# Kernel optimization log

Measured on AMD Instinct MI355X. Metric: run time of the kernel, lower is better.

The kernel has to match this reference:

```python
import jax, jax.numpy as jnp
import numpy as np

B = 128          # graphs per batch
NP = 1024        # nodes per graph
FIN = 128        # input node features
H = 128          # hidden width (SAGEConv out)
C = 10           # output classes
N = B * NP
DEG = 16
E = N * DEG
K1 = int(np.ceil(0.8 * NP))   # 820
K2 = int(np.ceil(0.8 * K1))   # 656
K3 = int(np.ceil(0.8 * K2))   # 525


def setup_inputs() -> dict:
    key = jax.random.key(0)
    k = jax.random.split(key, 16)
    x = jax.random.normal(k[0], (N, FIN), jnp.float32)
    # edges constrained within each graph (PyG batched-graph semantics)
    g = jnp.arange(E, dtype=jnp.int32) // (E // B)
    src = g * NP + jax.random.randint(k[1], (E,), 0, NP, jnp.int32)
    dst = g * NP + jax.random.randint(k[2], (E,), 0, NP, jnp.int32)
    edge_index = jnp.stack([src, dst])

    def lin(kk, o, i):
        return jax.random.normal(kk, (o, i), jnp.float32) / np.sqrt(i)

    return {
        'x': x, 'edge_index': edge_index,
        'Wl1': lin(k[3], H, FIN), 'bl1': jnp.zeros((H,), jnp.float32), 'Wr1': lin(k[4], H, FIN),
        'wp1': jax.random.normal(k[5], (H,), jnp.float32),
        'Wl2': lin(k[6], H, H), 'bl2': jnp.zeros((H,), jnp.float32), 'Wr2': lin(k[7], H, H),
        'wp2': jax.random.normal(k[8], (H,), jnp.float32),
        'Wl3': lin(k[9], H, H), 'bl3': jnp.zeros((H,), jnp.float32), 'Wr3': lin(k[10], H, H),
        'wp3': jax.random.normal(k[11], (H,), jnp.float32),
        'Wf1': lin(k[12], 64, H), 'bf1': jnp.zeros((64,), jnp.float32),
        'Wf2': lin(k[13], C, 64), 'bf2': jnp.zeros((C,), jnp.float32),
    }


def _sage(x, src, dst, em, Wl, bl, Wr):
    # PyG SAGEConv: lin_l(mean_{j in N(i)} x_j) + lin_r(x_i); edge mask em kills pruned edges
    msg = x[src] * em[:, None]                                   # [E,H] gather
    s = jax.ops.segment_sum(msg, dst, num_segments=N)            # scatter-add
    deg = jax.ops.segment_sum(em, dst, num_segments=N)
    mean = s / jnp.maximum(deg, 1.0)[:, None]
    return mean @ Wl.T + bl + x @ Wr.T


def _topk(x, w, nm, kk):
    # TopKPooling: score = x.w/||w||, keep top ceil(ratio*n) per graph, gate kept nodes by tanh(score)
    score = (x @ w) / (jnp.linalg.norm(w) + 1e-16)               # [N]
    s2 = jnp.where(nm, score, -jnp.inf).reshape(B, NP)
    _, idx = jax.lax.top_k(s2, kk)                               # [B,kk] static shape
    sel = jnp.zeros((B, NP), bool).at[jnp.arange(B)[:, None], idx].set(True).reshape(-1)
    x = jnp.where(sel[:, None], x * jnp.tanh(score)[:, None], 0.0)
    return x, sel


def _forward(x, Wl1, bl1, Wr1, wp1, Wl2, bl2, Wr2, wp2, Wl3, bl3, Wr3, wp3,
             Wf1, bf1, Wf2, bf2, edge_index):
    src, dst = edge_index[0], edge_index[1]
    nm = jnp.ones((N,), bool)                 # node alive mask
    em = jnp.ones((E,), jnp.float32)          # edge alive mask
    for (Wl, bl, Wr, wp, kk) in ((Wl1, bl1, Wr1, wp1, K1),
                                 (Wl2, bl2, Wr2, wp2, K2),
                                 (Wl3, bl3, Wr3, wp3, K3)):
        x = jax.nn.relu(_sage(x, src, dst, em, Wl, bl, Wr))
        x, nm = _topk(x, wp, nm, kk)
        em = (nm[src] & nm[dst]).astype(jnp.float32)
    # global_mean_pool over surviving nodes per graph (pruned nodes are exactly zero)
    cnt = nm.reshape(B, NP).sum(1).astype(x.dtype)
    pooled = x.reshape(B, NP, H).sum(1) / jnp.maximum(cnt, 1.0)[:, None]
    h = jax.nn.relu(pooled @ Wf1.T + bf1)
    return jax.nn.log_softmax(h @ Wf2.T + bf2, axis=-1)


def reference(x, edge_index, Wl1, bl1, Wr1, wp1, Wl2, bl2, Wr2, wp2,
              Wl3, bl3, Wr3, wp3, Wf1, bf1, Wf2, bf2):
    return _forward(x, Wl1, bl1, Wr1, wp1, Wl2, bl2, Wr2, wp2,
                    Wl3, bl3, Wr3, wp3, Wf1, bf1, Wf2, bf2, edge_index)
```

## Files before the change

kernel.cpp:

```cpp
#include <hip/hip_runtime.h>

constexpr int NGPH = 128;
constexpr int NPG  = 1024;
constexpr int NN   = NGPH * NPG;
constexpr int HD   = 128;
constexpr int EPG  = 16384;
constexpr int KS1 = 820, KS2 = 656, KS3 = 525;

typedef _Float16 half4v __attribute__((ext_vector_type(4)));
typedef _Float16 half8v __attribute__((ext_vector_type(8)));
typedef float f32x4 __attribute__((ext_vector_type(4)));

__global__ __launch_bounds__(256) void init_gate(float* __restrict__ gate) {
  int i = blockIdx.x * 256 + threadIdx.x;
  if (i < NN) gate[i] = 1.0f;
}

__global__ __launch_bounds__(512) void csr_build(int* __restrict__ ei) {
  __shared__ unsigned int ed[EPG];
  __shared__ int cnt[NPG];
  __shared__ int scn[NPG];
  __shared__ int off[NPG];
  int g = blockIdx.x, t = threadIdx.x;
  const int* srcg = ei + (size_t)g * EPG;
  const int* dstg = ei + (size_t)NGPH * EPG + (size_t)g * EPG;
  for (int i = t; i < EPG; i += 512) {
    unsigned int s = (unsigned int)(srcg[i] - (g << 10));
    unsigned int d = (unsigned int)(dstg[i] - (g << 10));
    ed[i] = s | (d << 10);
  }
  for (int i = t; i < NPG; i += 512) cnt[i] = 0;
  __syncthreads();
  for (int i = t; i < EPG; i += 512) atomicAdd(&cnt[ed[i] >> 10], 1);
  __syncthreads();
  int* a = cnt; int* b = scn;
  for (int d = 1; d < NPG; d <<= 1) {
    for (int i = t; i < NPG; i += 512) b[i] = a[i] + (i >= d ? a[i - d] : 0);
    __syncthreads();
    int* tmp = a; a = b; b = tmp;
  }
  unsigned short* ssort = (unsigned short*)(ei + (size_t)g * EPG);
  unsigned short* rsout = ssort + EPG;
  for (int r = t; r < NPG; r += 512) {
    int ex = r ? a[r - 1] : 0;
    rsout[r] = (unsigned short)ex;
    off[r] = ex;
  }
  __syncthreads();
  for (int i = t; i < EPG; i += 512) {
    unsigned int e = ed[i];
    int pos = atomicAdd(&off[e >> 10], 1);
    ssort[pos] = (unsigned short)(e & 1023u);
  }
}

__global__ __launch_bounds__(256) void agg2_kernel(const float* __restrict__ X,
                                                   const int* __restrict__ ei,
                                                   const float* __restrict__ gate,
                                                   float* __restrict__ Mout) {
  int t = threadIdx.x;
  int xcd = blockIdx.x & 7, q = blockIdx.x >> 3;
  int g = ((q >> 7) << 3) + xcd;
  int r = (q & 127) * 8 + (t >> 5);
  int lane = t & 31;
  const unsigned short* ss  = (const unsigned short*)(ei + (size_t)g * EPG);
  const unsigned short* rsg = ss + EPG;
  int start = rsg[r];
  int end   = (r < 1023) ? (int)rsg[r + 1] : EPG;
  const float4* X4 = (const float4*)X;
  size_t gb4 = (size_t)(g << 10) * 32;
  float4 acc = make_float4(0.f, 0.f, 0.f, 0.f);
  float degf = 0.f;
  for (int base = start; base < end; base += 32) {
    int ec = end - base; if (ec > 32) ec = 32;
    int sl = 0; float gv = 0.f;
    if (lane < ec) {
      sl = ss[base + lane];
      gv = gate[(g << 10) + sl];
    }
    degf += (gv != 0.f) ? 1.f : 0.f;
    int e = 0;
    for (; e + 4 <= ec; e += 4) {
      int s0 = __shfl(sl, e, 32),     s1 = __shfl(sl, e + 1, 32);
      int s2 = __shfl(sl, e + 2, 32), s3 = __shfl(sl, e + 3, 32);
      float g0 = __shfl(gv, e, 32),     g1 = __shfl(gv, e + 1, 32);
      float g2 = __shfl(gv, e + 2, 32), g3 = __shfl(gv, e + 3, 32);
      float4 v0 = X4[gb4 + (size_t)s0 * 32 + lane];
      float4 v1 = X4[gb4 + (size_t)s1 * 32 + lane];
      float4 v2 = X4[gb4 + (size_t)s2 * 32 + lane];
      float4 v3 = X4[gb4 + (size_t)s3 * 32 + lane];
      acc.x += v0.x * g0 + v1.x * g1 + v2.x * g2 + v3.x * g3;
      acc.y += v0.y * g0 + v1.y * g1 + v2.y * g2 + v3.y * g3;
      acc.z += v0.z * g0 + v1.z * g1 + v2.z * g2 + v3.z * g3;
      acc.w += v0.w * g0 + v1.w * g1 + v2.w * g2 + v3.w * g3;
    }
    for (; e < ec; ++e) {
      int s0 = __shfl(sl, e, 32);
      float g0 = __shfl(gv, e, 32);
      float4 v0 = X4[gb4 + (size_t)s0 * 32 + lane];
      acc.x += v0.x * g0; acc.y += v0.y * g0;
      acc.z += v0.z * g0; acc.w += v0.w * g0;
    }
  }
#pragma unroll
  for (int m = 1; m <= 16; m <<= 1) degf += __shfl_xor(degf, m, 32);
  float inv = 1.0f / fmaxf(degf, 1.0f);
  acc.x *= inv; acc.y *= inv; acc.z *= inv; acc.w *= inv;
  ((float4*)Mout)[(size_t)((g << 10) + r) * 32 + lane] = acc;
}

constexpr int LDA = 40;
__global__ __launch_bounds__(256) void gemm_mfma(const float* S,
                                                 const float* __restrict__ X,
                                                 const float* __restrict__ Wl,
                                                 const float* __restrict__ Wr,
                                                 const float* __restrict__ bb,
                                                 const float* __restrict__ wp,
                                                 const float* __restrict__ gate,
                                                 float* Hout,
                                                 float* __restrict__ score) {
  __shared__ _Float16 Ah[128 * LDA];
  __shared__ _Float16 Al[128 * LDA];
  __shared__ _Float16 Bh[128 * LDA];
  __shared__ _Float16 Bl[128 * LDA];
  __shared__ float sc_s[128];
  int t = threadIdx.x;
  int r0 = blockIdx.x * 128;
  int lane = t & 63, wid = t >> 6;
  int wm = wid & 1, wn = wid >> 1;
  int quad = lane >> 4, mr = lane & 15;

  f32x4 acc[4][4];
#pragma unroll
  for (int i = 0; i < 4; ++i)
#pragma unroll
    for (int j = 0; j < 4; ++j) acc[i][j] = (f32x4){0.f, 0.f, 0.f, 0.f};

  for (int ks = 0; ks < 256; ks += 32) {
    bool isS = (ks < 128);
    const float* Asrc = isS ? (S + (size_t)r0 * HD + ks)
                            : (X + (size_t)r0 * HD + (ks - 128));
#pragma unroll
    for (int i = 0; i < 4; ++i) {
      int f = t + i * 256;
      int row = f >> 3;
      int kq = (f & 7) * 4;
      float4 v = *(const float4*)&Asrc[(size_t)row * HD + kq];
      if (!isS) {
        float gv = gate[r0 + row];
        v.x *= gv; v.y *= gv; v.z *= gv; v.w *= gv;
      }
      half4v h, l;
      h.x = (_Float16)v.x; h.y = (_Float16)v.y; h.z = (_Float16)v.z; h.w = (_Float16)v.w;
      l.x = (_Float16)(v.x - (float)h.x); l.y = (_Float16)(v.y - (float)h.y);
      l.z = (_Float16)(v.z - (float)h.z); l.w = (_Float16)(v.w - (float)h.w);
      *(half4v*)&Ah[row * LDA + kq] = h;
      *(half4v*)&Al[row * LDA + kq] = l;
    }
    const float* Wsrc = isS ? (Wl + ks) : (Wr + (ks - 128));
#pragma unroll
    for (int i = 0; i < 4; ++i) {
      int f = t + i * 256;
      int row = f >> 3;
      int kq = (f & 7) * 4;
      float4 v = *(const float4*)&Wsrc[(size_t)row * HD + kq];
      half4v h, l;
      h.x = (_Float16)v.x; h.y = (_Float16)v.y; h.z = (_Float16)v.z; h.w = (_Float16)v.w;
      l.x = (_Float16)(v.x - (float)h.x); l.y = (_Float16)(v.y - (float)h.y);
      l.z = (_Float16)(v.z - (float)h.z); l.w = (_Float16)(v.w - (float)h.w);
      *(half4v*)&Bh[row * LDA + kq] = h;
      *(half4v*)&Bl[row * LDA + kq] = l;
    }
    __syncthreads();
    half8v af[4], alf[4], bf[4], blf[4];
#pragma unroll
    for (int i = 0; i < 4; ++i) {
      int rowA = (wm * 64 + i * 16 + mr) * LDA + quad * 8;
      af[i]  = *(const half8v*)&Ah[rowA];
      alf[i] = *(const half8v*)&Al[rowA];
    }
#pragma unroll
    for (int j = 0; j < 4; ++j) {
      int rowW = (wn * 64 + j * 16 + mr) * LDA + quad * 8;
      bf[j]  = *(const half8v*)&Bh[rowW];
      blf[j] = *(const half8v*)&Bl[rowW];
    }
#pragma unroll
    for (int i = 0; i < 4; ++i)
#pragma unroll
      for (int j = 0; j < 4; ++j) {
        acc[i][j] = __builtin_amdgcn_mfma_f32_16x16x32_f16(af[i],  bf[j],  acc[i][j], 0, 0, 0);
        acc[i][j] = __builtin_amdgcn_mfma_f32_16x16x32_f16(af[i],  blf[j], acc[i][j], 0, 0, 0);
        acc[i][j] = __builtin_amdgcn_mfma_f32_16x16x32_f16(alf[i], bf[j],  acc[i][j], 0, 0, 0);
      }
    __syncthreads();
  }
  if (t < 128) sc_s[t] = 0.f;
  __syncthreads();
  float p[4][4];
#pragma unroll
  for (int i = 0; i < 4; ++i)
#pragma unroll
    for (int r = 0; r < 4; ++r) p[i][r] = 0.f;
#pragma unroll
  for (int j = 0; j < 4; ++j) {
    int col = wn * 64 + j * 16 + mr;
    float bias = bb[col];
    float wv = wp[col];
#pragma unroll
    for (int i = 0; i < 4; ++i) {
      int rowg = r0 + wm * 64 + i * 16 + quad * 4;
#pragma unroll
      for (int r = 0; r < 4; ++r) {
        float ho = fmaxf(acc[i][j][r] + bias, 0.f);
        Hout[(size_t)(rowg + r) * HD + col] = ho;
        p[i][r] += ho * wv;
      }
    }
  }
#pragma unroll
  for (int i = 0; i < 4; ++i)
#pragma unroll
    for (int r = 0; r < 4; ++r) {
#pragma unroll
      for (int m = 1; m <= 8; m <<= 1) p[i][r] += __shfl_xor(p[i][r], m, 16);
      if (mr == 0) atomicAdd(&sc_s[wm * 64 + i * 16 + quad * 4 + r], p[i][r]);
    }
  __syncthreads();
  if (t < 128) score[r0 + t] = sc_s[t];
}

__global__ __launch_bounds__(256) void topk_kernel(const float* __restrict__ score,
                                                   float* __restrict__ gate,
                                                   const float* __restrict__ wp,
                                                   int kk) {
  __shared__ float sc[NPG];
  __shared__ float srt[NPG];
  __shared__ float shv[1];
  int g = blockIdx.x, t = threadIdx.x;
  if (t == 0) {
    float ss = 0.f;
    for (int i = 0; i < HD; ++i) ss += wp[i] * wp[i];
    shv[0] = 1.0f / (sqrtf(ss) + 1e-16f);
  }
  __syncthreads();
  float inv = shv[0];
#pragma unroll
  for (int q = 0; q < 4; ++q) {
    int n = t + q * 256;
    float s = score[(g << 10) + n] * inv;
    sc[n] = s;
    srt[n] = (gate[(g << 10) + n] != 0.f) ? s : -3.402823466e38f;
  }
  __syncthreads();
  for (int k2 = 2; k2 <= NPG; k2 <<= 1) {
    for (int j = k2 >> 1; j > 0; j >>= 1) {
#pragma unroll
      for (int q = 0; q < 4; ++q) {
        int i = t + q * 256;
        int l = i ^ j;
        if (l > i) {
          float a = srt[i], b = srt[l];
          if ((a > b) == ((i & k2) == 0)) { srt[i] = b; srt[l] = a; }
        }
      }
      __syncthreads();
    }
  }
  float thr = srt[NPG - kk];
#pragma unroll
  for (int q = 0; q < 4; ++q) {
    int n = t + q * 256;
    float s = sc[n];
    bool sel = (gate[(g << 10) + n] != 0.f) && (s >= thr);
    gate[(g << 10) + n] = sel ? tanhf(s) : 0.f;
  }
}

__global__ __launch_bounds__(128) void final_kernel(const float* __restrict__ X,
                                                    const float* __restrict__ gate,
                                                    const float* __restrict__ Wf1,
                                                    const float* __restrict__ bf1,
                                                    const float* __restrict__ Wf2,
                                                    const float* __restrict__ bf2,
                                                    float* __restrict__ out) {
  __shared__ float gs[NPG];
  __shared__ float pl[HD];
  __shared__ float h1[64];
  __shared__ float lg[10];
  __shared__ float red[2];
  int g = blockIdx.x, t = threadIdx.x;
  for (int i = t; i < NPG; i += 128) gs[i] = gate[(g << 10) + i];
  __syncthreads();
  size_t base = (size_t)g * NPG * HD;
  float s = 0.f;
  for (int r = 0; r < NPG; ++r) s += X[base + (size_t)r * HD + t] * gs[r];
  pl[t] = s / (float)KS3;
  __syncthreads();
  if (t < 64) {
    float h = bf1[t];
    for (int f = 0; f < HD; ++f) h += pl[f] * Wf1[t * HD + f];
    h1[t] = fmaxf(h, 0.f);
  }
  __syncthreads();
  if (t < 10) {
    float z = bf2[t];
    for (int j = 0; j < 64; ++j) z += h1[j] * Wf2[t * 64 + j];
    lg[t] = z;
  }
  __syncthreads();
  if (t == 0) {
    float m = lg[0];
    for (int c = 1; c < 10; ++c) m = fmaxf(m, lg[c]);
    float ssum = 0.f;
    for (int c = 0; c < 10; ++c) ssum += expf(lg[c] - m);
    red[0] = m; red[1] = logf(ssum);
  }
  __syncthreads();
  if (t < 10) out[g * 10 + t] = lg[t] - red[0] - red[1];
}

extern "C" void kernel_launch(void* const* d_in, const int* in_sizes, int n_in,
                              void* d_out, int out_size, void* d_ws, size_t ws_size,
                              hipStream_t stream) {
  const float* x  = (const float*)d_in[0];
  int* ei         = (int*)d_in[1];
  const float* Wl[3]  = {(const float*)d_in[2], (const float*)d_in[6],  (const float*)d_in[10]};
  const float* blv[3] = {(const float*)d_in[3], (const float*)d_in[7],  (const float*)d_in[11]};
  const float* Wr[3]  = {(const float*)d_in[4], (const float*)d_in[8],  (const float*)d_in[12]};
  const float* wp[3]  = {(const float*)d_in[5], (const float*)d_in[9],  (const float*)d_in[13]};
  const float* Wf1 = (const float*)d_in[14];
  const float* bf1 = (const float*)d_in[15];
  const float* Wf2 = (const float*)d_in[16];
  const float* bf2 = (const float*)d_in[17];
  float* out = (float*)d_out;

  float* bufA  = (float*)d_ws;
  float* bufB  = bufA + (size_t)NN * HD;
  float* gate  = bufB + (size_t)NN * HD;
  float* score = gate + NN;

  init_gate<<<NN / 256, 256, 0, stream>>>(gate);
  csr_build<<<NGPH, 512, 0, stream>>>(ei);

  agg2_kernel<<<NN / 8, 256, 0, stream>>>(x, ei, gate, bufA);
  gemm_mfma<<<NN / 128, 256, 0, stream>>>(bufA, x, Wl[0], Wr[0], blv[0], wp[0], gate, bufA, score);
  topk_kernel<<<NGPH, 256, 0, stream>>>(score, gate, wp[0], KS1);
  agg2_kernel<<<NN / 8, 256, 0, stream>>>(bufA, ei, gate, bufB);
  gemm_mfma<<<NN / 128, 256, 0, stream>>>(bufB, bufA, Wl[1], Wr[1], blv[1], wp[1], gate, bufB, score);
  topk_kernel<<<NGPH, 256, 0, stream>>>(score, gate, wp[1], KS2);
  agg2_kernel<<<NN / 8, 256, 0, stream>>>(bufB, ei, gate, bufA);
  gemm_mfma<<<NN / 128, 256, 0, stream>>>(bufA, bufB, Wl[2], Wr[2], blv[2], wp[2], gate, bufA, score);
  topk_kernel<<<NGPH, 256, 0, stream>>>(score, gate, wp[2], KS3);

  final_kernel<<<NGPH, 128, 0, stream>>>(bufA, gate, Wf1, bf1, Wf2, bf2, out);
}
```

Before: 562.6 us.

## Pre-split weights to fp16 hi/lo, widen aggregation unroll, parallelize final pooling

```diff
diff --git a/kernel.cpp b/kernel.cpp
--- a/kernel.cpp
+++ b/kernel.cpp
@@ -7,13 +7,30 @@
 constexpr int EPG  = 16384;
 constexpr int KS1 = 820, KS2 = 656, KS3 = 525;
 
-typedef _Float16 half4v __attribute__((ext_vector_type(4)));
 typedef _Float16 half8v __attribute__((ext_vector_type(8)));
 typedef float f32x4 __attribute__((ext_vector_type(4)));
 
 __global__ __launch_bounds__(256) void init_gate(float* __restrict__ gate) {
   int i = blockIdx.x * 256 + threadIdx.x;
   if (i < NN) gate[i] = 1.0f;
+}
+
+__global__ __launch_bounds__(256) void wconv(const float* __restrict__ Wl0, const float* __restrict__ Wr0,
+                                             const float* __restrict__ Wl1, const float* __restrict__ Wr1,
+                                             const float* __restrict__ Wl2, const float* __restrict__ Wr2,
+                                             _Float16* __restrict__ Wc) {
+  int tid = blockIdx.x * 256 + threadIdx.x;
+  int layer = tid >> 15;
+  int idx = tid & 32767;
+  int n = idx >> 8, k = idx & 255;
+  const float* Wlp = layer == 0 ? Wl0 : layer == 1 ? Wl1 : Wl2;
+  const float* Wrp = layer == 0 ? Wr0 : layer == 1 ? Wr1 : Wr2;
+  float v = (k < 128) ? Wlp[n * 128 + k] : Wrp[n * 128 + k - 128];
+  _Float16 h = (_Float16)v;
+  _Float16 l = (_Float16)(v - (float)h);
+  size_t base = (size_t)layer * 65536;
+  Wc[base + (size_t)n * 256 + k] = h;
+  Wc[base + 32768 + (size_t)n * 256 + k] = l;
 }
 
 __global__ __launch_bounds__(512) void csr_build(int* __restrict__ ei) {
@@ -80,19 +97,29 @@
     }
     degf += (gv != 0.f) ? 1.f : 0.f;
     int e = 0;
+    for (; e + 8 <= ec; e += 8) {
+      int s[8]; float gg[8]; float4 v[8];
+#pragma unroll
+      for (int k = 0; k < 8; ++k) { s[k] = __shfl(sl, e + k, 32); gg[k] = __shfl(gv, e + k, 32); }
+#pragma unroll
+      for (int k = 0; k < 8; ++k) v[k] = X4[gb4 + (size_t)s[k] * 32 + lane];
+#pragma unroll
+      for (int k = 0; k < 8; ++k) {
+        acc.x += v[k].x * gg[k]; acc.y += v[k].y * gg[k];
+        acc.z += v[k].z * gg[k]; acc.w += v[k].w * gg[k];
+      }
+    }
     for (; e + 4 <= ec; e += 4) {
-      int s0 = __shfl(sl, e, 32),     s1 = __shfl(sl, e + 1, 32);
-      int s2 = __shfl(sl, e + 2, 32), s3 = __shfl(sl, e + 3, 32);
-      float g0 = __shfl(gv, e, 32),     g1 = __shfl(gv, e + 1, 32);
-      float g2 = __shfl(gv, e + 2, 32), g3 = __shfl(gv, e + 3, 32);
-      float4 v0 = X4[gb4 + (size_t)s0 * 32 + lane];
-      float4 v1 = X4[gb4 + (size_t)s1 * 32 + lane];
-      float4 v2 = X4[gb4 + (size_t)s2 * 32 + lane];
-      float4 v3 = X4[gb4 + (size_t)s3 * 32 + lane];
-      acc.x += v0.x * g0 + v1.x * g1 + v2.x * g2 + v3.x * g3;
-      acc.y += v0.y * g0 + v1.y * g1 + v2.y * g2 + v3.y * g3;
-      acc.z += v0.z * g0 + v1.z * g1 + v2.z * g2 + v3.z * g3;
-      acc.w += v0.w * g0 + v1.w * g1 + v2.w * g2 + v3.w * g3;
+      int s[4]; float gg[4]; float4 v[4];
+#pragma unroll
+      for (int k = 0; k < 4; ++k) { s[k] = __shfl(sl, e + k, 32); gg[k] = __shfl(gv, e + k, 32); }
+#pragma unroll
+      for (int k = 0; k < 4; ++k) v[k] = X4[gb4 + (size_t)s[k] * 32 + lane];
+#pragma unroll
+      for (int k = 0; k < 4; ++k) {
+        acc.x += v[k].x * gg[k]; acc.y += v[k].y * gg[k];
+        acc.z += v[k].z * gg[k]; acc.w += v[k].w * gg[k];
+      }
     }
     for (; e < ec; ++e) {
       int s0 = __shfl(sl, e, 32);
@@ -109,16 +136,15 @@
   ((float4*)Mout)[(size_t)((g << 10) + r) * 32 + lane] = acc;
 }
 
-constexpr int LDA = 40;
-__global__ __launch_bounds__(256) void gemm_mfma(const float* S,
-                                                 const float* __restrict__ X,
-                                                 const float* __restrict__ Wl,
-                                                 const float* __restrict__ Wr,
-                                                 const float* __restrict__ bb,
-                                                 const float* __restrict__ wp,
-                                                 const float* __restrict__ gate,
-                                                 float* Hout,
-                                                 float* __restrict__ score) {
+constexpr int LDA = 34;
+__global__ __launch_bounds__(256, 4) void gemm_mfma(const float* S,
+                                                    const float* __restrict__ X,
+                                                    const _Float16* __restrict__ Wc,
+                                                    const float* __restrict__ bb,
+                                                    const float* __restrict__ wp,
+                                                    const float* __restrict__ gate,
+                                                    float* Hout,
+                                                    float* __restrict__ score) {
   __shared__ _Float16 Ah[128 * LDA];
   __shared__ _Float16 Al[128 * LDA];
   __shared__ _Float16 Bh[128 * LDA];
@@ -129,6 +155,8 @@
   int lane = t & 63, wid = t >> 6;
   int wm = wid & 1, wn = wid >> 1;
   int quad = lane >> 4, mr = lane & 15;
+  const _Float16* WH = Wc;
+  const _Float16* WL = Wc + 32768;
 
   f32x4 acc[4][4];
 #pragma unroll
@@ -141,35 +169,34 @@
     const float* Asrc = isS ? (S + (size_t)r0 * HD + ks)
                             : (X + (size_t)r0 * HD + (ks - 128));
 #pragma unroll
-    for (int i = 0; i < 4; ++i) {
-      int f = t + i * 256;
-      int row = f >> 3;
-      int kq = (f & 7) * 4;
-      float4 v = *(const float4*)&Asrc[(size_t)row * HD + kq];
+    for (int i = 0; i < 2; ++i) {
+      int slot = t + i * 256;
+      int row = slot >> 2;
+      int kq = (slot & 3) * 8;
+      float4 v0 = *(const float4*)&Asrc[(size_t)row * HD + kq];
+      float4 v1 = *(const float4*)&Asrc[(size_t)row * HD + kq + 4];
       if (!isS) {
         float gv = gate[r0 + row];
-        v.x *= gv; v.y *= gv; v.z *= gv; v.w *= gv;
-      }
-      half4v h, l;
-      h.x = (_Float16)v.x; h.y = (_Float16)v.y; h.z = (_Float16)v.z; h.w = (_Float16)v.w;
-      l.x = (_Float16)(v.x - (float)h.x); l.y = (_Float16)(v.y - (float)h.y);
-      l.z = (_Float16)(v.z - (float)h.z); l.w = (_Float16)(v.w - (float)h.w);
-      *(half4v*)&Ah[row * LDA + kq] = h;
-      *(half4v*)&Al[row * LDA + kq] = l;
-    }
-    const float* Wsrc = isS ? (Wl + ks) : (Wr + (ks - 128));
-#pragma unroll
-    for (int i = 0; i < 4; ++i) {
-      int f = t + i * 256;
-      int row = f >> 3;
-      int kq = (f & 7) * 4;
-      float4 v = *(const float4*)&Wsrc[(size_t)row * HD + kq];
-      half4v h, l;
-      h.x = (_Float16)v.x; h.y = (_Float16)v.y; h.z = (_Float16)v.z; h.w = (_Float16)v.w;
-      l.x = (_Float16)(v.x - (float)h.x); l.y = (_Float16)(v.y - (float)h.y);
-      l.z = (_Float16)(v.z - (float)h.z); l.w = (_Float16)(v.w - (float)h.w);
-      *(half4v*)&Bh[row * LDA + kq] = h;
-      *(half4v*)&Bl[row * LDA + kq] = l;
+        v0.x *= gv; v0.y *= gv; v0.z *= gv; v0.w *= gv;
+        v1.x *= gv; v1.y *= gv; v1.z *= gv; v1.w *= gv;
+      }
+      half8v h, l;
+      h[0] = (_Float16)v0.x; h[1] = (_Float16)v0.y; h[2] = (_Float16)v0.z; h[3] = (_Float16)v0.w;
+      h[4] = (_Float16)v1.x; h[5] = (_Float16)v1.y; h[6] = (_Float16)v1.z; h[7] = (_Float16)v1.w;
+      l[0] = (_Float16)(v0.x - (float)h[0]); l[1] = (_Float16)(v0.y - (float)h[1]);
+      l[2] = (_Float16)(v0.z - (float)h[2]); l[3] = (_Float16)(v0.w - (float)h[3]);
+      l[4] = (_Float16)(v1.x - (float)h[4]); l[5] = (_Float16)(v1.y - (float)h[5]);
+      l[6] = (_Float16)(v1.z - (float)h[6]); l[7] = (_Float16)(v1.w - (float)h[7]);
+      *(half8v*)&Ah[row * LDA + kq] = h;
+      *(half8v*)&Al[row * LDA + kq] = l;
+    }
+#pragma unroll
+    for (int i = 0; i < 2; ++i) {
+      int slot = t + i * 256;
+      int n = slot >> 2;
+      int kq = (slot & 3) * 8;
+      *(half8v*)&Bh[n * LDA + kq] = *(const half8v*)&WH[(size_t)n * 256 + ks + kq];
+      *(half8v*)&Bl[n * LDA + kq] = *(const half8v*)&WL[(size_t)n * 256 + ks + kq];
     }
     __syncthreads();
     half8v af[4], alf[4], bf[4], blf[4];
@@ -277,29 +304,39 @@
   }
 }
 
-__global__ __launch_bounds__(128) void final_kernel(const float* __restrict__ X,
-                                                    const float* __restrict__ gate,
-                                                    const float* __restrict__ Wf1,
-                                                    const float* __restrict__ bf1,
-                                                    const float* __restrict__ Wf2,
-                                                    const float* __restrict__ bf2,
-                                                    float* __restrict__ out) {
+__global__ __launch_bounds__(1024) void final_kernel(const float* __restrict__ X,
+                                                     const float* __restrict__ gate,
+                                                     const float* __restrict__ Wf1,
+                                                     const float* __restrict__ bf1,
+                                                     const float* __restrict__ Wf2,
+                                                     const float* __restrict__ bf2,
+                                                     float* __restrict__ out) {
   __shared__ float gs[NPG];
+  __shared__ float ps[8][HD];
   __shared__ float pl[HD];
   __shared__ float h1[64];
   __shared__ float lg[10];
   __shared__ float red[2];
   int g = blockIdx.x, t = threadIdx.x;
-  for (int i = t; i < NPG; i += 128) gs[i] = gate[(g << 10) + i];
-  __syncthreads();
+  gs[t] = gate[(g << 10) + t];
+  __syncthreads();
+  int c = t >> 7, f = t & 127;
   size_t base = (size_t)g * NPG * HD;
   float s = 0.f;
-  for (int r = 0; r < NPG; ++r) s += X[base + (size_t)r * HD + t] * gs[r];
-  pl[t] = s / (float)KS3;
+  for (int r = c * 128; r < c * 128 + 128; ++r)
+    s += X[base + (size_t)r * HD + f] * gs[r];
+  ps[c][f] = s;
+  __syncthreads();
+  if (t < HD) {
+    float tot = 0.f;
+#pragma unroll
+    for (int cc = 0; cc < 8; ++cc) tot += ps[cc][t];
+    pl[t] = tot / (float)KS3;
+  }
   __syncthreads();
   if (t < 64) {
     float h = bf1[t];
-    for (int f = 0; f < HD; ++f) h += pl[f] * Wf1[t * HD + f];
+    for (int ff = 0; ff < HD; ++ff) h += pl[ff] * Wf1[t * HD + ff];
     h1[t] = fmaxf(h, 0.f);
   }
   __syncthreads();
@@ -311,9 +348,9 @@
   __syncthreads();
   if (t == 0) {
     float m = lg[0];
-    for (int c = 1; c < 10; ++c) m = fmaxf(m, lg[c]);
+    for (int cc = 1; cc < 10; ++cc) m = fmaxf(m, lg[cc]);
     float ssum = 0.f;
-    for (int c = 0; c < 10; ++c) ssum += expf(lg[c] - m);
+    for (int cc = 0; cc < 10; ++cc) ssum += expf(lg[cc] - m);
     red[0] = m; red[1] = logf(ssum);
   }
   __syncthreads();
@@ -339,19 +376,21 @@
   float* bufB  = bufA + (size_t)NN * HD;
   float* gate  = bufB + (size_t)NN * HD;
   float* score = gate + NN;
+  _Float16* Wcvt = (_Float16*)(score + NN);
 
   init_gate<<<NN / 256, 256, 0, stream>>>(gate);
+  wconv<<<384, 256, 0, stream>>>(Wl[0], Wr[0], Wl[1], Wr[1], Wl[2], Wr[2], Wcvt);
   csr_build<<<NGPH, 512, 0, stream>>>(ei);
 
   agg2_kernel<<<NN / 8, 256, 0, stream>>>(x, ei, gate, bufA);
-  gemm_mfma<<<NN / 128, 256, 0, stream>>>(bufA, x, Wl[0], Wr[0], blv[0], wp[0], gate, bufA, score);
+  gemm_mfma<<<NN / 128, 256, 0, stream>>>(bufA, x, Wcvt, blv[0], wp[0], gate, bufA, score);
   topk_kernel<<<NGPH, 256, 0, stream>>>(score, gate, wp[0], KS1);
   agg2_kernel<<<NN / 8, 256, 0, stream>>>(bufA, ei, gate, bufB);
-  gemm_mfma<<<NN / 128, 256, 0, stream>>>(bufB, bufA, Wl[1], Wr[1], blv[1], wp[1], gate, bufB, score);
+  gemm_mfma<<<NN / 128, 256, 0, stream>>>(bufB, bufA, Wcvt + 65536, blv[1], wp[1], gate, bufB, score);
   topk_kernel<<<NGPH, 256, 0, stream>>>(score, gate, wp[1], KS2);
   agg2_kernel<<<NN / 8, 256, 0, stream>>>(bufB, ei, gate, bufA);
-  gemm_mfma<<<NN / 128, 256, 0, stream>>>(bufA, bufB, Wl[2], Wr[2], blv[2], wp[2], gate, bufA, score);
+  gemm_mfma<<<NN / 128, 256, 0, stream>>>(bufA, bufB, Wcvt + 131072, blv[2], wp[2], gate, bufA, score);
   topk_kernel<<<NGPH, 256, 0, stream>>>(score, gate, wp[2], KS3);
 
-  final_kernel<<<NGPH, 128, 0, stream>>>(bufA, gate, Wf1, bf1, Wf2, bf2, out);
-}
+  final_kernel<<<NGPH, 1024, 0, stream>>>(bufA, gate, Wf1, bf1, Wf2, bf2, out);
+}
```

Result: slower. 591.3 us (+5.1%).

## Widen CSR build, double GEMM k-step, split final pooling across more blocks

Applied to the files above, without the earlier changes.

```diff
diff --git a/kernel.cpp b/kernel.cpp
--- a/kernel.cpp
+++ b/kernel.cpp
@@ -7,7 +7,6 @@
 constexpr int EPG  = 16384;
 constexpr int KS1 = 820, KS2 = 656, KS3 = 525;
 
-typedef _Float16 half4v __attribute__((ext_vector_type(4)));
 typedef _Float16 half8v __attribute__((ext_vector_type(8)));
 typedef float f32x4 __attribute__((ext_vector_type(4)));
 
@@ -16,41 +15,37 @@
   if (i < NN) gate[i] = 1.0f;
 }
 
-__global__ __launch_bounds__(512) void csr_build(int* __restrict__ ei) {
-  __shared__ unsigned int ed[EPG];
+__global__ __launch_bounds__(1024) void csr_build(int* __restrict__ ei) {
+  __shared__ unsigned short sloc[EPG];
   __shared__ int cnt[NPG];
   __shared__ int scn[NPG];
   __shared__ int off[NPG];
   int g = blockIdx.x, t = threadIdx.x;
   const int* srcg = ei + (size_t)g * EPG;
   const int* dstg = ei + (size_t)NGPH * EPG + (size_t)g * EPG;
-  for (int i = t; i < EPG; i += 512) {
-    unsigned int s = (unsigned int)(srcg[i] - (g << 10));
-    unsigned int d = (unsigned int)(dstg[i] - (g << 10));
-    ed[i] = s | (d << 10);
-  }
-  for (int i = t; i < NPG; i += 512) cnt[i] = 0;
-  __syncthreads();
-  for (int i = t; i < EPG; i += 512) atomicAdd(&cnt[ed[i] >> 10], 1);
+  cnt[t] = 0;
+  for (int i = t; i < EPG; i += 1024)
+    sloc[i] = (unsigned short)(srcg[i] - (g << 10));
+  __syncthreads();
+  for (int i = t; i < EPG; i += 1024)
+    atomicAdd(&cnt[dstg[i] - (g << 10)], 1);
   __syncthreads();
   int* a = cnt; int* b = scn;
   for (int d = 1; d < NPG; d <<= 1) {
-    for (int i = t; i < NPG; i += 512) b[i] = a[i] + (i >= d ? a[i - d] : 0);
+    b[t] = a[t] + (t >= d ? a[t - d] : 0);
     __syncthreads();
     int* tmp = a; a = b; b = tmp;
   }
   unsigned short* ssort = (unsigned short*)(ei + (size_t)g * EPG);
   unsigned short* rsout = ssort + EPG;
-  for (int r = t; r < NPG; r += 512) {
-    int ex = r ? a[r - 1] : 0;
-    rsout[r] = (unsigned short)ex;
-    off[r] = ex;
-  }
-  __syncthreads();
-  for (int i = t; i < EPG; i += 512) {
-    unsigned int e = ed[i];
-    int pos = atomicAdd(&off[e >> 10], 1);
-    ssort[pos] = (unsigned short)(e & 1023u);
+  int ex = t ? a[t - 1] : 0;
+  rsout[t] = (unsigned short)ex;
+  off[t] = ex;
+  __syncthreads();
+  for (int i = t; i < EPG; i += 1024) {
+    int d = dstg[i] - (g << 10);
+    int pos = atomicAdd(&off[d], 1);
+    ssort[pos] = sloc[i];
   }
 }
 
@@ -109,7 +104,7 @@
   ((float4*)Mout)[(size_t)((g << 10) + r) * 32 + lane] = acc;
 }
 
-constexpr int LDA = 40;
+constexpr int LDA = 72;
 __global__ __launch_bounds__(256) void gemm_mfma(const float* S,
                                                  const float* __restrict__ X,
                                                  const float* __restrict__ Wl,
@@ -136,63 +131,76 @@
 #pragma unroll
     for (int j = 0; j < 4; ++j) acc[i][j] = (f32x4){0.f, 0.f, 0.f, 0.f};
 
-  for (int ks = 0; ks < 256; ks += 32) {
+  for (int ks = 0; ks < 256; ks += 64) {
     bool isS = (ks < 128);
     const float* Asrc = isS ? (S + (size_t)r0 * HD + ks)
                             : (X + (size_t)r0 * HD + (ks - 128));
+    const float* Wsrc = isS ? (Wl + ks) : (Wr + (ks - 128));
 #pragma unroll
     for (int i = 0; i < 4; ++i) {
-      int f = t + i * 256;
-      int row = f >> 3;
-      int kq = (f & 7) * 4;
-      float4 v = *(const float4*)&Asrc[(size_t)row * HD + kq];
+      int slot = t + i * 256;
+      int row = slot >> 3;
+      int kq = (slot & 7) * 8;
+      float4 v0 = *(const float4*)&Asrc[(size_t)row * HD + kq];
+      float4 v1 = *(const float4*)&Asrc[(size_t)row * HD + kq + 4];
       if (!isS) {
         float gv = gate[r0 + row];
-        v.x *= gv; v.y *= gv; v.z *= gv; v.w *= gv;
-      }
-      half4v h, l;
-      h.x = (_Float16)v.x; h.y = (_Float16)v.y; h.z = (_Float16)v.z; h.w = (_Float16)v.w;
-      l.x = (_Float16)(v.x - (float)h.x); l.y = (_Float16)(v.y - (float)h.y);
-      l.z = (_Float16)(v.z - (float)h.z); l.w = (_Float16)(v.w - (float)h.w);
-      *(half4v*)&Ah[row * LDA + kq] = h;
-      *(half4v*)&Al[row * LDA + kq] = l;
-    }
-    const float* Wsrc = isS ? (Wl + ks) : (Wr + (ks - 128));
+        v0.x *= gv; v0.y *= gv; v0.z *= gv; v0.w *= gv;
+        v1.x *= gv; v1.y *= gv; v1.z *= gv; v1.w *= gv;
+      }
+      half8v h, l;
+      h[0] = (_Float16)v0.x; h[1] = (_Float16)v0.y; h[2] = (_Float16)v0.z; h[3] = (_Float16)v0.w;
+      h[4] = (_Float16)v1.x; h[5] = (_Float16)v1.y; h[6] = (_Float16)v1.z; h[7] = (_Float16)v1.w;
+      l[0] = (_Float16)(v0.x - (float)h[0]); l[1] = (_Float16)(v0.y - (float)h[1]);
+      l[2] = (_Float16)(v0.z - (float)h[2]); l[3] = (_Float16)(v0.w - (float)h[3]);
+      l[4] = (_Float16)(v1.x - (float)h[4]); l[5] = (_Float16)(v1.y - (float)h[5]);
+      l[6] = (_Float16)(v1.z - (float)h[6]); l[7] = (_Float16)(v1.w - (float)h[7]);
+      *(half8v*)&Ah[row * LDA + kq] = h;
+      *(half8v*)&Al[row * LDA + kq] = l;
+    }
 #pragma unroll
     for (int i = 0; i < 4; ++i) {
-      int f = t + i * 256;
-      int row = f >> 3;
-      int kq = (f & 7) * 4;
-      float4 v = *(const float4*)&Wsrc[(size_t)row * HD + kq];
-      half4v h, l;
-      h.x = (_Float16)v.x; h.y = (_Float16)v.y; h.z = (_Float16)v.z; h.w = (_Float16)v.w;
-      l.x = (_Float16)(v.x - (float)h.x); l.y = (_Float16)(v.y - (float)h.y);
-      l.z = (_Float16)(v.z - (float)h.z); l.w = (_Float16)(v.w - (float)h.w);
-      *(half4v*)&Bh[row * LDA + kq] = h;
-      *(half4v*)&Bl[row * LDA + kq] = l;
+      int slot = t + i * 256;
+      int n = slot >> 3;
+      int kq = (slot & 7) * 8;
+      float4 v0 = *(const float4*)&Wsrc[(size_t)n * HD + kq];
+      float4 v1 = *(const float4*)&Wsrc[(size_t)n * HD + kq + 4];
+      half8v h, l;
+      h[0] = (_Float16)v0.x; h[1] = (_Float16)v0.y; h[2] = (_Float16)v0.z; h[3] = (_Float16)v0.w;
+      h[4] = (_Float16)v1.x; h[5] = (_Float16)v1.y; h[6] = (_Float16)v1.z; h[7] = (_Float16)v1.w;
+      l[0] = (_Float16)(v0.x - (float)h[0]); l[1] = (_Float16)(v0.y - (float)h[1]);
+      l[2] = (_Float16)(v0.z - (float)h[2]); l[3] = (_Float16)(v0.w - (float)h[3]);
+      l[4] = (_Float16)(v1.x - (float)h[4]); l[5] = (_Float16)(v1.y - (float)h[5]);
+      l[6] = (_Float16)(v1.z - (float)h[6]); l[7] = (_Float16)(v1.w - (float)h[7]);
+      *(half8v*)&Bh[n * LDA + kq] = h;
+      *(half8v*)&Bl[n * LDA + kq] = l;
     }
     __syncthreads();
-    half8v af[4], alf[4], bf[4], blf[4];
-#pragma unroll
-    for (int i = 0; i < 4; ++i) {
-      int rowA = (wm * 64 + i * 16 + mr) * LDA + quad * 8;
-      af[i]  = *(const half8v*)&Ah[rowA];
-      alf[i] = *(const half8v*)&Al[rowA];
-    }
-#pragma unroll
-    for (int j = 0; j < 4; ++j) {
-      int rowW = (wn * 64 + j * 16 + mr) * LDA + quad * 8;
-      bf[j]  = *(const half8v*)&Bh[rowW];
-      blf[j] = *(const half8v*)&Bl[rowW];
-    }
-#pragma unroll
-    for (int i = 0; i < 4; ++i)
+#pragma unroll
+    for (int su = 0; su < 2; ++su) {
+      int ko = su * 32;
+      half8v af[4], alf[4], bf[4], blf[4];
+#pragma unroll
+      for (int i = 0; i < 4; ++i) {
+        int rowA = (wm * 64 + i * 16 + mr) * LDA + ko + quad * 8;
+        af[i]  = *(const half8v*)&Ah[rowA];
+        alf[i] = *(const half8v*)&Al[rowA];
+      }
 #pragma unroll
       for (int j = 0; j < 4; ++j) {
-        acc[i][j] = __builtin_amdgcn_mfma_f32_16x16x32_f16(af[i],  bf[j],  acc[i][j], 0, 0, 0);
-        acc[i][j] = __builtin_amdgcn_mfma_f32_16x16x32_f16(af[i],  blf[j], acc[i][j], 0, 0, 0);
-        acc[i][j] = __builtin_amdgcn_mfma_f32_16x16x32_f16(alf[i], bf[j],  acc[i][j], 0, 0, 0);
-      }
+        int rowW = (wn * 64 + j * 16 + mr) * LDA + ko + quad * 8;
+        bf[j]  = *(const half8v*)&Bh[rowW];
+        blf[j] = *(const half8v*)&Bl[rowW];
+      }
+#pragma unroll
+      for (int i = 0; i < 4; ++i)
+#pragma unroll
+        for (int j = 0; j < 4; ++j) {
+          acc[i][j] = __builtin_amdgcn_mfma_f32_16x16x32_f16(af[i],  bf[j],  acc[i][j], 0, 0, 0);
+          acc[i][j] = __builtin_amdgcn_mfma_f32_16x16x32_f16(af[i],  blf[j], acc[i][j], 0, 0, 0);
+          acc[i][j] = __builtin_amdgcn_mfma_f32_16x16x32_f16(alf[i], bf[j],  acc[i][j], 0, 0, 0);
+        }
+    }
     __syncthreads();
   }
   if (t < 128) sc_s[t] = 0.f;
@@ -277,29 +285,45 @@
   }
 }
 
-__global__ __launch_bounds__(128) void final_kernel(const float* __restrict__ X,
+__global__ __launch_bounds__(256) void pool1_kernel(const float* __restrict__ X,
                                                     const float* __restrict__ gate,
-                                                    const float* __restrict__ Wf1,
-                                                    const float* __restrict__ bf1,
-                                                    const float* __restrict__ Wf2,
-                                                    const float* __restrict__ bf2,
-                                                    float* __restrict__ out) {
-  __shared__ float gs[NPG];
+                                                    float* __restrict__ part) {
+  __shared__ float gs[128];
+  __shared__ float ps[2][HD];
+  int b = blockIdx.x;
+  int g = b >> 3, c = b & 7;
+  int t = threadIdx.x;
+  if (t < 128) gs[t] = gate[(g << 10) + c * 128 + t];
+  __syncthreads();
+  int f = t & 127, sub = t >> 7;
+  size_t base = (size_t)((g << 10) + c * 128) * HD;
+  float s = 0.f;
+  for (int r = sub; r < 128; r += 2)
+    s += X[base + (size_t)r * HD + f] * gs[r];
+  ps[sub][f] = s;
+  __syncthreads();
+  if (t < 128) part[(g << 10) + c * 128 + t] = ps[0][t] + ps[1][t];
+}
+
+__global__ __launch_bounds__(128) void final2_kernel(const float* __restrict__ part,
+                                                     const float* __restrict__ Wf1,
+                                                     const float* __restrict__ bf1,
+                                                     const float* __restrict__ Wf2,
+                                                     const float* __restrict__ bf2,
+                                                     float* __restrict__ out) {
   __shared__ float pl[HD];
   __shared__ float h1[64];
   __shared__ float lg[10];
   __shared__ float red[2];
   int g = blockIdx.x, t = threadIdx.x;
-  for (int i = t; i < NPG; i += 128) gs[i] = gate[(g << 10) + i];
-  __syncthreads();
-  size_t base = (size_t)g * NPG * HD;
-  float s = 0.f;
-  for (int r = 0; r < NPG; ++r) s += X[base + (size_t)r * HD + t] * gs[r];
-  pl[t] = s / (float)KS3;
+  float tot = 0.f;
+#pragma unroll
+  for (int c = 0; c < 8; ++c) tot += part[(g << 10) + c * 128 + t];
+  pl[t] = tot / (float)KS3;
   __syncthreads();
   if (t < 64) {
     float h = bf1[t];
-    for (int f = 0; f < HD; ++f) h += pl[f] * Wf1[t * HD + f];
+    for (int ff = 0; ff < HD; ++ff) h += pl[ff] * Wf1[t * HD + ff];
     h1[t] = fmaxf(h, 0.f);
   }
   __syncthreads();
@@ -311,9 +335,9 @@
   __syncthreads();
   if (t == 0) {
     float m = lg[0];
-    for (int c = 1; c < 10; ++c) m = fmaxf(m, lg[c]);
+    for (int cc = 1; cc < 10; ++cc) m = fmaxf(m, lg[cc]);
     float ssum = 0.f;
-    for (int c = 0; c < 10; ++c) ssum += expf(lg[c] - m);
+    for (int cc = 0; cc < 10; ++cc) ssum += expf(lg[cc] - m);
     red[0] = m; red[1] = logf(ssum);
   }
   __syncthreads();
@@ -341,7 +365,7 @@
   float* score = gate + NN;
 
   init_gate<<<NN / 256, 256, 0, stream>>>(gate);
-  csr_build<<<NGPH, 512, 0, stream>>>(ei);
+  csr_build<<<NGPH, 1024, 0, stream>>>(ei);
 
   agg2_kernel<<<NN / 8, 256, 0, stream>>>(x, ei, gate, bufA);
   gemm_mfma<<<NN / 128, 256, 0, stream>>>(bufA, x, Wl[0], Wr[0], blv[0], wp[0], gate, bufA, score);
@@ -353,5 +377,6 @@
   gemm_mfma<<<NN / 128, 256, 0, stream>>>(bufA, bufB, Wl[2], Wr[2], blv[2], wp[2], gate, bufA, score);
   topk_kernel<<<NGPH, 256, 0, stream>>>(score, gate, wp[2], KS3);
 
-  final_kernel<<<NGPH, 128, 0, stream>>>(bufA, gate, Wf1, bf1, Wf2, bf2, out);
-}
+  pool1_kernel<<<NGPH * 8, 256, 0, stream>>>(bufA, gate, score);
+  final2_kernel<<<NGPH, 128, 0, stream>>>(score, Wf1, bf1, Wf2, bf2, out);
+}
```

New measurement: 572.1 us. Within noise of the previous version (+1.7%).
